# Kernel tuning notes

Hardware: AMD Instinct MI355X
Metric: run time of the kernel (lower is better)

Reference implementation:

```python
import jax, jax.numpy as jnp
import numpy as np

TEMPERATURE = 0.5
BN_EPS = 1e-5
L2_EPS = 1e-12

B, D_IN, D_HID, D_OUT = 4096, 192, 512, 128


def setup_inputs() -> dict:
    key = jax.random.key(0)
    ks = jax.random.split(key, 4)
    return {
        "h1": jax.random.normal(ks[0], (B, D_IN), dtype=jnp.float32),
        "h2": jax.random.normal(ks[1], (B, D_IN), dtype=jnp.float32),
        "W1": jax.random.normal(ks[2], (D_HID, D_IN), dtype=jnp.float32) * (1.0 / np.sqrt(D_IN)),
        "b1": jnp.zeros((D_HID,), dtype=jnp.float32),
        "gamma": jnp.ones((D_HID,), dtype=jnp.float32),
        "beta": jnp.zeros((D_HID,), dtype=jnp.float32),
        "W2": jax.random.normal(ks[3], (D_OUT, D_HID), dtype=jnp.float32) * (1.0 / np.sqrt(D_HID)),
        "b2": jnp.zeros((D_OUT,), dtype=jnp.float32),
    }


def _projection_head(h, W1, b1, gamma, beta, W2, b2):
    # Linear -> BatchNorm1d (training-mode batch stats) -> ReLU -> Linear
    y = h @ W1.T + b1  # (B, D_HID)
    mean = jnp.mean(y, axis=0)
    var = jnp.mean((y - mean) ** 2, axis=0)  # biased var, as torch BN uses for normalization
    y = (y - mean) * jax.lax.rsqrt(var + BN_EPS) * gamma + beta
    y = jax.nn.relu(y)
    return y @ W2.T + b2  # (B, D_OUT)


def _l2_normalize(z):
    n = jnp.sqrt(jnp.sum(z * z, axis=1, keepdims=True))
    return z / jnp.maximum(n, L2_EPS)


def reference(h1, h2, W1, b1, gamma, beta, W2, b2):
    z1 = _l2_normalize(_projection_head(h1, W1, b1, gamma, beta, W2, b2))
    z2 = _l2_normalize(_projection_head(h2, W1, b1, gamma, beta, W2, b2))

    # NT-Xent, fully vectorized (equivalent to the per-row torch loop):
    z = jnp.concatenate([z1, z2], axis=0)            # (2B, D)
    sim = (z @ z.T) / TEMPERATURE                    # (2B, 2B)
    n2 = z.shape[0]
    sim = jnp.where(jnp.eye(n2, dtype=bool), -jnp.inf, sim)
    # positive pair similarity: sim[i, i+B] and sim[i+B, i] == z1_i . z2_i / T
    pos = jnp.sum(z1 * z2, axis=1) / TEMPERATURE     # (B,)
    pos = jnp.concatenate([pos, pos])                # (2B,)
    # excluding index i from the row equals including it since diag is -inf
    lse = jax.nn.logsumexp(sim, axis=1)              # (2B,)
    loss = jnp.mean(lse - pos)
    return loss, z1, z2
```

## Files before the change

kernel.cpp:

```cpp
#include <hip/hip_runtime.h>


#define NB   4096
#define DIN  192
#define DHID 512
#define DOUT 128
#define N2   8192
#define NSPLIT 32
#define SIM_ITERS 16

typedef short short8 __attribute__((ext_vector_type(8)));
typedef float floatx4 __attribute__((ext_vector_type(4)));

__device__ inline float fast_exp2(float x) {
#if __has_builtin(__builtin_amdgcn_exp2f)
    return __builtin_amdgcn_exp2f(x);
#else
    return exp2f(x);
#endif
}

__device__ inline unsigned short bf16_rne(float x) {
    unsigned int u = __float_as_uint(x);
    return (unsigned short)((u + 0x7fffu + ((u >> 16) & 1u)) >> 16);
}

__global__ __launch_bounds__(256) void convert_w(
    const float* __restrict__ W1, const float* __restrict__ W2,
    unsigned short* __restrict__ W1b, unsigned short* __restrict__ W2b)
{
    const int NW1 = DHID * DIN / 4;
    const int NW2 = DOUT * DHID / 4;
    int id = blockIdx.x * 256 + threadIdx.x;
    const float* src; unsigned short* dst; int off;
    if (id < NW1)            { src = W1; dst = W1b; off = id; }
    else if (id < NW1 + NW2) { src = W2; dst = W2b; off = id - NW1; }
    else return;
    float4 x = ((const float4*)src)[off];
    unsigned int p0 = bf16_rne(x.x) | ((unsigned int)bf16_rne(x.y) << 16);
    unsigned int p1 = bf16_rne(x.z) | ((unsigned int)bf16_rne(x.w) << 16);
    ((uint2*)dst)[off] = make_uint2(p0, p1);
}

__global__ __launch_bounds__(256) void gemm1_mfma(
    const float* __restrict__ h1, const float* __restrict__ h2,
    const unsigned short* __restrict__ W1b, const float* __restrict__ b1,
    float* __restrict__ Y, float* __restrict__ psumc, float* __restrict__ psqc)
{
    const int t = threadIdx.x;
    const int wave = t >> 6, lane = t & 63;
    const int quad = lane >> 4, l15 = lane & 15;
    const int mb = blockIdx.x;
    const int m0 = mb * 128 + wave * 32;
    const int n0 = blockIdx.y * 64;
    const int v  = (mb >= 32);

    short8 a[2][6];
    #pragma unroll
    for (int mt = 0; mt < 2; ++mt) {
        int row = m0 + mt * 16 + l15;
        const float* hsrc = (row < NB) ? (h1 + (size_t)row * DIN)
                                       : (h2 + (size_t)(row - NB) * DIN);
        #pragma unroll
        for (int kc = 0; kc < 6; ++kc) {
            const float4* p = (const float4*)(hsrc + kc * 32 + quad * 8);
            float4 x0 = p[0], x1 = p[1];
            float xs[8] = {x0.x,x0.y,x0.z,x0.w,x1.x,x1.y,x1.z,x1.w};
            #pragma unroll
            for (int j = 0; j < 8; ++j) a[mt][kc][j] = (short)bf16_rne(xs[j]);
        }
    }

    #pragma unroll
    for (int nt = 0; nt < 4; ++nt) {
        const int col = n0 + nt * 16 + l15;
        const short8* bptr = (const short8*)(W1b + (size_t)col * DIN + quad * 8);
        short8 b[6];
        #pragma unroll
        for (int kc = 0; kc < 6; ++kc) b[kc] = bptr[kc * 4];
        floatx4 acc[2] = {{0.f,0.f,0.f,0.f},{0.f,0.f,0.f,0.f}};
        #pragma unroll
        for (int kc = 0; kc < 6; ++kc)
            #pragma unroll
            for (int mt = 0; mt < 2; ++mt)
                acc[mt] = __builtin_amdgcn_mfma_f32_16x16x32_bf16(a[mt][kc], b[kc], acc[mt], 0,0,0);
        const float bias = b1[col];
        float cs = 0.f, cq = 0.f;
        #pragma unroll
        for (int mt = 0; mt < 2; ++mt)
            #pragma unroll
            for (int reg = 0; reg < 4; ++reg) {
                float y = acc[mt][reg] + bias;
                int row = m0 + mt * 16 + quad * 4 + reg;
                Y[(size_t)row * DHID + col] = y;
                cs += y; cq += y * y;
            }
        cs += __shfl_xor(cs, 16); cs += __shfl_xor(cs, 32);
        cq += __shfl_xor(cq, 16); cq += __shfl_xor(cq, 32);
        if (quad == 0) {
            atomicAdd(psumc + v * DHID + col, cs);
            atomicAdd(psqc  + v * DHID + col, cq);
        }
    }
}

#define ZSCALE 1.6986436f

__global__ __launch_bounds__(256) void gemm2_mfma(
    const float* __restrict__ Y, const unsigned short* __restrict__ W2b,
    const float* __restrict__ psumc, const float* __restrict__ psqc,
    const float* __restrict__ gamma, const float* __restrict__ beta,
    const float* __restrict__ b2,
    unsigned short* __restrict__ Zb, float* __restrict__ outz)
{
    __shared__ float sc_sh[DHID], sh_sh[DHID];
    __shared__ float sq_lds[4][16];
    const int t = threadIdx.x;
    const int wave = t >> 6, lane = t & 63;
    const int quad = lane >> 4, l15 = lane & 15;
    const int mtbase = blockIdx.x * 16;
    const int v = (mtbase >= NB);

    for (int c = t; c < DHID; c += 256) {
        float mean = psumc[v * DHID + c] * (1.0f / NB);
        float var  = psqc [v * DHID + c] * (1.0f / NB) - mean * mean;
        float rstd = rsqrtf(var + 1e-5f);
        float scv = gamma[c] * rstd;
        sc_sh[c] = scv;
        sh_sh[c] = beta[c] - mean * scv;
    }
    __syncthreads();

    const float* yrow = Y + (size_t)(mtbase + l15) * DHID;
    floatx4 acc[2] = {{0.f,0.f,0.f,0.f},{0.f,0.f,0.f,0.f}};
    for (int kc = 0; kc < 16; ++kc) {
        const int k = kc * 32 + quad * 8;
        float4 y0 = *(const float4*)(yrow + k);
        float4 y1 = *(const float4*)(yrow + k + 4);
        float4 s0 = *(const float4*)&sc_sh[k], s1 = *(const float4*)&sc_sh[k + 4];
        float4 h0 = *(const float4*)&sh_sh[k], h1v = *(const float4*)&sh_sh[k + 4];
        float xs[8];
        xs[0] = fmaxf(y0.x * s0.x + h0.x, 0.f);
        xs[1] = fmaxf(y0.y * s0.y + h0.y, 0.f);
        xs[2] = fmaxf(y0.z * s0.z + h0.z, 0.f);
        xs[3] = fmaxf(y0.w * s0.w + h0.w, 0.f);
        xs[4] = fmaxf(y1.x * s1.x + h1v.x, 0.f);
        xs[5] = fmaxf(y1.y * s1.y + h1v.y, 0.f);
        xs[6] = fmaxf(y1.z * s1.z + h1v.z, 0.f);
        xs[7] = fmaxf(y1.w * s1.w + h1v.w, 0.f);
        short8 a;
        #pragma unroll
        for (int j = 0; j < 8; ++j) a[j] = (short)bf16_rne(xs[j]);
        #pragma unroll
        for (int nt = 0; nt < 2; ++nt) {
            const int col = wave * 32 + nt * 16 + l15;
            short8 b = *(const short8*)(W2b + (size_t)col * DHID + k);
            acc[nt] = __builtin_amdgcn_mfma_f32_16x16x32_bf16(a, b, acc[nt], 0,0,0);
        }
    }
    float bias[2];
    #pragma unroll
    for (int nt = 0; nt < 2; ++nt) bias[nt] = b2[wave * 32 + nt * 16 + l15];

    float zv[4][2];
    #pragma unroll
    for (int reg = 0; reg < 4; ++reg) {
        float sq = 0.f;
        #pragma unroll
        for (int nt = 0; nt < 2; ++nt) {
            zv[reg][nt] = acc[nt][reg] + bias[nt];
            sq += zv[reg][nt] * zv[reg][nt];
        }
        sq += __shfl_xor(sq, 1); sq += __shfl_xor(sq, 2);
        sq += __shfl_xor(sq, 4); sq += __shfl_xor(sq, 8);
        if (l15 == 0) sq_lds[wave][quad * 4 + reg] = sq;
    }
    __syncthreads();
    #pragma unroll
    for (int reg = 0; reg < 4; ++reg) {
        float tot = sq_lds[0][quad * 4 + reg] + sq_lds[1][quad * 4 + reg]
                  + sq_lds[2][quad * 4 + reg] + sq_lds[3][quad * 4 + reg];
        float inv = 1.0f / fmaxf(sqrtf(tot), 1e-12f);
        const int row = mtbase + quad * 4 + reg;
        const size_t ob = (size_t)row * DOUT;
        #pragma unroll
        for (int nt = 0; nt < 2; ++nt) {
            const int col = wave * 32 + nt * 16 + l15;
            float z = zv[reg][nt] * inv;
            outz[ob + col] = z;
            Zb[ob + col] = bf16_rne(z * ZSCALE);
        }
    }
}

__global__ __launch_bounds__(256, 2) void sim_mfma(
    const unsigned short* __restrict__ Zb, float* __restrict__ psum)
{
    __shared__ unsigned char bsh[65536];
    const int t = threadIdx.x;
    const int wave = t >> 6, lane = t & 63;
    const int quad = lane >> 4, l15 = lane & 15;
    const int mbase = blockIdx.x * 128 + wave * 32;
    const int cs = blockIdx.y;
    const int cbase = cs * (N2 / NSPLIT);

    {
        const uint4* src = (const uint4*)(Zb + (size_t)cbase * DOUT);
        #pragma unroll
        for (int k = 0; k < 16; ++k) {
            int idx = t + k * 256;
            uint4 vv = src[idx];
            int row  = idx >> 4;
            int slot = idx & 15;
            *(uint4*)(bsh + row * 256 + ((slot ^ (row & 15)) << 4)) = vv;
        }
    }

    short8 a[2][4];
    #pragma unroll
    for (int at = 0; at < 2; ++at) {
        const short8* zra = (const short8*)(Zb + (size_t)(mbase + at * 16 + l15) * DOUT + quad * 8);
        #pragma unroll
        for (int kc = 0; kc < 4; ++kc) a[at][kc] = zra[kc * 4];
    }

    float rs[2][4];
    #pragma unroll
    for (int at = 0; at < 2; ++at)
        #pragma unroll
        for (int r = 0; r < 4; ++r) rs[at][r] = 0.f;

    __syncthreads();

    #pragma unroll 1
    for (int nt = 0; nt < SIM_ITERS; ++nt) {
        const int crow = nt * 16 + l15;
        short8 b[4];
        #pragma unroll
        for (int kc = 0; kc < 4; ++kc) {
            int slot = kc * 4 + quad;
            int boff = crow * 256 + ((slot ^ (crow & 15)) << 4);
            b[kc] = *(const short8*)(bsh + boff);
        }

        floatx4 acc[2] = {{0.f,0.f,0.f,0.f},{0.f,0.f,0.f,0.f}};
        #pragma unroll
        for (int kc = 0; kc < 4; ++kc)
            #pragma unroll
            for (int at = 0; at < 2; ++at)
                acc[at] = __builtin_amdgcn_mfma_f32_16x16x32_bf16(a[at][kc], b[kc], acc[at], 0, 0, 0);

        #pragma unroll
        for (int at = 0; at < 2; ++at)
            #pragma unroll
            for (int r = 0; r < 4; ++r)
                rs[at][r] += fast_exp2(acc[at][r]);
    }

    #pragma unroll
    for (int at = 0; at < 2; ++at) {
        const int gi0 = mbase + at * 16 + quad * 4;
        #pragma unroll
        for (int r = 0; r < 4; ++r) {
            float s = rs[at][r];
            s += __shfl_xor(s, 1);
            s += __shfl_xor(s, 2);
            s += __shfl_xor(s, 4);
            s += __shfl_xor(s, 8);
            if (l15 == 0) psum[(size_t)cs * N2 + gi0 + r] = s;
        }
    }
}

__global__ __launch_bounds__(256) void row_finalize(
    const unsigned short* __restrict__ Zb, const float* __restrict__ psum,
    float* __restrict__ out)
{
    int i = blockIdx.x * 256 + threadIdx.x;
    float s = 0.f;
    #pragma unroll
    for (int cs = 0; cs < NSPLIT; ++cs) s += psum[(size_t)cs * N2 + i];
    int k = i & (NB - 1);
    const uint4* z1 = (const uint4*)(Zb + (size_t)k * DOUT);
    const uint4* z2 = (const uint4*)(Zb + (size_t)(k + NB) * DOUT);
    float d12 = 0.f, d11 = 0.f, d22 = 0.f;
    #pragma unroll
    for (int q = 0; q < 16; ++q) {
        uint4 a = z1[q], bqq = z2[q];
        const unsigned int aw[4] = {a.x, a.y, a.z, a.w};
        const unsigned int bw[4] = {bqq.x, bqq.y, bqq.z, bqq.w};
        #pragma unroll
        for (int c = 0; c < 4; ++c) {
            float alo = __uint_as_float(aw[c] << 16);
            float ahi = __uint_as_float(aw[c] & 0xffff0000u);
            float blo = __uint_as_float(bw[c] << 16);
            float bhi = __uint_as_float(bw[c] & 0xffff0000u);
            d12 += alo * blo + ahi * bhi;
            d11 += alo * alo + ahi * ahi;
            d22 += blo * blo + bhi * bhi;
        }
    }
    float dself = (i < NB) ? d11 : d22;
    float rowval = logf(s - fast_exp2(dself)) - d12 * 0.69314718f;

    float r = rowval;
    r += __shfl_xor(r, 1);  r += __shfl_xor(r, 2);  r += __shfl_xor(r, 4);
    r += __shfl_xor(r, 8);  r += __shfl_xor(r, 16); r += __shfl_xor(r, 32);
    __shared__ float wsr[4];
    int lane = threadIdx.x & 63, w = threadIdx.x >> 6;
    if (lane == 0) wsr[w] = r;
    __syncthreads();
    if (threadIdx.x == 0)
        atomicAdd(out, (wsr[0] + wsr[1] + wsr[2] + wsr[3]) * (1.0f / N2));
}

extern "C" void kernel_launch(void* const* d_in, const int* in_sizes, int n_in,
                              void* d_out, int out_size, void* d_ws, size_t ws_size,
                              hipStream_t stream)
{
    const float* h1    = (const float*)d_in[0];
    const float* h2    = (const float*)d_in[1];
    const float* W1    = (const float*)d_in[2];
    const float* b1    = (const float*)d_in[3];
    const float* gamma = (const float*)d_in[4];
    const float* beta  = (const float*)d_in[5];
    const float* W2    = (const float*)d_in[6];
    const float* b2    = (const float*)d_in[7];
    float* out = (float*)d_out;

    float* ws      = (float*)d_ws;
    float* psumc   = ws;
    float* psqc    = psumc + 1024;
    unsigned short* W1b = (unsigned short*)(psqc + 1024);
    unsigned short* W2b = W1b + DHID * DIN;
    float* Y       = (float*)(W2b + DOUT * DHID);
    float* psum    = Y + (size_t)N2 * DHID;
    unsigned short* Zb = (unsigned short*)(psum + (size_t)NSPLIT * N2);

    hipMemsetAsync(psumc, 0, 2048 * sizeof(float), stream);
    hipMemsetAsync(out, 0, sizeof(float), stream);

    convert_w   <<<dim3(160),        256, 0, stream>>>(W1, W2, W1b, W2b);
    gemm1_mfma  <<<dim3(64, 8),      256, 0, stream>>>(h1, h2, W1b, b1, Y, psumc, psqc);
    gemm2_mfma  <<<dim3(512),        256, 0, stream>>>(Y, W2b, psumc, psqc, gamma, beta, b2, Zb, out + 1);
    sim_mfma    <<<dim3(64, NSPLIT), 256, 0, stream>>>(Zb, psum);
    row_finalize<<<dim3(32),         256, 0, stream>>>(Zb, psum, out);
}
```

Baseline: 145.3 us.

## Fuse projection GEMMs into one cooperative kernel with grid sync for BN stats

Replaces the separate gemm1 and gemm2 launches with a single cooperative kernel. Each block computes a 16-row slice of the hidden activations into LDS, accumulates the BatchNorm column statistics atomically, grid-syncs, then applies BN, ReLU, the second GEMM and the L2 normalisation in place. This removes the round trip of the 8192x512 fp32 hidden activations through global memory and one launch. In exchange it needs all 512 blocks co-resident, adds a grid-wide barrier, and has each block recompute over a small tile with lower MFMA reuse of W1 and W2. If the cooperative launch fails it falls back to the old two-kernel path.

```diff
diff --git a/kernel.cpp b/kernel.cpp
--- a/kernel.cpp
+++ b/kernel.cpp
@@ -1,4 +1,5 @@
 #include <hip/hip_runtime.h>
+#include <hip/hip_cooperative_groups.h>
 
 
 #define NB   4096
@@ -42,6 +43,142 @@
     ((uint2*)dst)[off] = make_uint2(p0, p1);
 }
 
+#define ZSCALE 1.6986436f
+
+__global__ __launch_bounds__(256, 2) void fused_head(
+    const float* __restrict__ h1, const float* __restrict__ h2,
+    const unsigned short* __restrict__ W1b, const float* __restrict__ b1,
+    const unsigned short* __restrict__ W2b,
+    float* __restrict__ psumc, float* __restrict__ psqc,
+    const float* __restrict__ gamma, const float* __restrict__ beta,
+    const float* __restrict__ b2,
+    unsigned short* __restrict__ Zb, float* __restrict__ outz)
+{
+    __shared__ float ytile[16][516];
+    __shared__ float sc_sh[DHID], sh_sh[DHID];
+    __shared__ float sq_lds[4][16];
+
+    const int t = threadIdx.x;
+    const int wave = t >> 6, lane = t & 63;
+    const int quad = lane >> 4, l15 = lane & 15;
+    const int r0 = blockIdx.x * 16;
+    const int v  = (r0 >= NB);
+
+    {
+        short8 a1[6];
+        {
+            const int row = r0 + l15;
+            const float* hsrc = (row < NB) ? (h1 + (size_t)row * DIN)
+                                           : (h2 + (size_t)(row - NB) * DIN);
+            #pragma unroll
+            for (int kc = 0; kc < 6; ++kc) {
+                const float4* p = (const float4*)(hsrc + kc * 32 + quad * 8);
+                float4 x0 = p[0], x1 = p[1];
+                float xs[8] = {x0.x,x0.y,x0.z,x0.w,x1.x,x1.y,x1.z,x1.w};
+                #pragma unroll
+                for (int j = 0; j < 8; ++j) a1[kc][j] = (short)bf16_rne(xs[j]);
+            }
+        }
+        #pragma unroll
+        for (int nt = 0; nt < 8; ++nt) {
+            const int col = wave * 128 + nt * 16 + l15;
+            const short8* bptr = (const short8*)(W1b + (size_t)col * DIN + quad * 8);
+            floatx4 acc = {0.f, 0.f, 0.f, 0.f};
+            #pragma unroll
+            for (int kc = 0; kc < 6; ++kc)
+                acc = __builtin_amdgcn_mfma_f32_16x16x32_bf16(a1[kc], bptr[kc * 4], acc, 0, 0, 0);
+            const float bias = b1[col];
+            float cs = 0.f, cq = 0.f;
+            #pragma unroll
+            for (int reg = 0; reg < 4; ++reg) {
+                float y = acc[reg] + bias;
+                ytile[quad * 4 + reg][col] = y;
+                cs += y; cq += y * y;
+            }
+            cs += __shfl_xor(cs, 16); cs += __shfl_xor(cs, 32);
+            cq += __shfl_xor(cq, 16); cq += __shfl_xor(cq, 32);
+            if (quad == 0) {
+                atomicAdd(psumc + v * DHID + col, cs);
+                atomicAdd(psqc  + v * DHID + col, cq);
+            }
+        }
+    }
+    __threadfence();
+    cooperative_groups::this_grid().sync();
+
+    for (int c = t; c < DHID; c += 256) {
+        float sm = __hip_atomic_load(psumc + v * DHID + c, __ATOMIC_RELAXED, __HIP_MEMORY_SCOPE_AGENT);
+        float sq = __hip_atomic_load(psqc  + v * DHID + c, __ATOMIC_RELAXED, __HIP_MEMORY_SCOPE_AGENT);
+        float mean = sm * (1.0f / NB);
+        float var  = sq * (1.0f / NB) - mean * mean;
+        float rstd = rsqrtf(var + 1e-5f);
+        float scv = gamma[c] * rstd;
+        sc_sh[c] = scv;
+        sh_sh[c] = beta[c] - mean * scv;
+    }
+    __syncthreads();
+
+    floatx4 acc2[2] = {{0.f,0.f,0.f,0.f},{0.f,0.f,0.f,0.f}};
+    for (int kc = 0; kc < 16; ++kc) {
+        const int k = kc * 32 + quad * 8;
+        float4 y0 = *(const float4*)&ytile[l15][k];
+        float4 y1 = *(const float4*)&ytile[l15][k + 4];
+        float4 s0 = *(const float4*)&sc_sh[k], s1 = *(const float4*)&sc_sh[k + 4];
+        float4 h0 = *(const float4*)&sh_sh[k], h1v = *(const float4*)&sh_sh[k + 4];
+        float xs[8];
+        xs[0] = fmaxf(y0.x * s0.x + h0.x, 0.f);
+        xs[1] = fmaxf(y0.y * s0.y + h0.y, 0.f);
+        xs[2] = fmaxf(y0.z * s0.z + h0.z, 0.f);
+        xs[3] = fmaxf(y0.w * s0.w + h0.w, 0.f);
+        xs[4] = fmaxf(y1.x * s1.x + h1v.x, 0.f);
+        xs[5] = fmaxf(y1.y * s1.y + h1v.y, 0.f);
+        xs[6] = fmaxf(y1.z * s1.z + h1v.z, 0.f);
+        xs[7] = fmaxf(y1.w * s1.w + h1v.w, 0.f);
+        short8 a;
+        #pragma unroll
+        for (int j = 0; j < 8; ++j) a[j] = (short)bf16_rne(xs[j]);
+        #pragma unroll
+        for (int nt = 0; nt < 2; ++nt) {
+            const int col = wave * 32 + nt * 16 + l15;
+            short8 b = *(const short8*)(W2b + (size_t)col * DHID + k);
+            acc2[nt] = __builtin_amdgcn_mfma_f32_16x16x32_bf16(a, b, acc2[nt], 0, 0, 0);
+        }
+    }
+    float bias2[2];
+    #pragma unroll
+    for (int nt = 0; nt < 2; ++nt) bias2[nt] = b2[wave * 32 + nt * 16 + l15];
+
+    float zv[4][2];
+    #pragma unroll
+    for (int reg = 0; reg < 4; ++reg) {
+        float sq = 0.f;
+        #pragma unroll
+        for (int nt = 0; nt < 2; ++nt) {
+            zv[reg][nt] = acc2[nt][reg] + bias2[nt];
+            sq += zv[reg][nt] * zv[reg][nt];
+        }
+        sq += __shfl_xor(sq, 1); sq += __shfl_xor(sq, 2);
+        sq += __shfl_xor(sq, 4); sq += __shfl_xor(sq, 8);
+        if (l15 == 0) sq_lds[wave][quad * 4 + reg] = sq;
+    }
+    __syncthreads();
+    #pragma unroll
+    for (int reg = 0; reg < 4; ++reg) {
+        float tot = sq_lds[0][quad * 4 + reg] + sq_lds[1][quad * 4 + reg]
+                  + sq_lds[2][quad * 4 + reg] + sq_lds[3][quad * 4 + reg];
+        float inv = 1.0f / fmaxf(sqrtf(tot), 1e-12f);
+        const int row = r0 + quad * 4 + reg;
+        const size_t ob = (size_t)row * DOUT;
+        #pragma unroll
+        for (int nt = 0; nt < 2; ++nt) {
+            const int col = wave * 32 + nt * 16 + l15;
+            float z = zv[reg][nt] * inv;
+            outz[ob + col] = z;
+            Zb[ob + col] = bf16_rne(z * ZSCALE);
+        }
+    }
+}
+
 __global__ __launch_bounds__(256) void gemm1_mfma(
     const float* __restrict__ h1, const float* __restrict__ h2,
     const unsigned short* __restrict__ W1b, const float* __restrict__ b1,
@@ -103,8 +240,6 @@
         }
     }
 }
-
-#define ZSCALE 1.6986436f
 
 __global__ __launch_bounds__(256) void gemm2_mfma(
     const float* __restrict__ Y, const unsigned short* __restrict__ W2b,
@@ -341,8 +476,26 @@
     hipMemsetAsync(out, 0, sizeof(float), stream);
 
     convert_w   <<<dim3(160),        256, 0, stream>>>(W1, W2, W1b, W2b);
-    gemm1_mfma  <<<dim3(64, 8),      256, 0, stream>>>(h1, h2, W1b, b1, Y, psumc, psqc);
-    gemm2_mfma  <<<dim3(512),        256, 0, stream>>>(Y, W2b, psumc, psqc, gamma, beta, b2, Zb, out + 1);
+
+    {
+        const unsigned short* W1b_c = W1b;
+        const unsigned short* W2b_c = W2b;
+        unsigned short* Zb_p = Zb;
+        float* outz = out + 1;
+        void* args[] = {
+            (void*)&h1, (void*)&h2, (void*)&W1b_c, (void*)&b1, (void*)&W2b_c,
+            (void*)&psumc, (void*)&psqc, (void*)&gamma, (void*)&beta,
+            (void*)&b2, (void*)&Zb_p, (void*)&outz
+        };
+        hipError_t ce = hipLaunchCooperativeKernel((void*)fused_head,
+                                                   dim3(512), dim3(256),
+                                                   args, 0, stream);
+        if (ce != hipSuccess) {
+            gemm1_mfma<<<dim3(64, 8), 256, 0, stream>>>(h1, h2, W1b, b1, Y, psumc, psqc);
+            gemm2_mfma<<<dim3(512),   256, 0, stream>>>(Y, W2b, psumc, psqc, gamma, beta, b2, Zb, out + 1);
+        }
+    }
+
     sim_mfma    <<<dim3(64, NSPLIT), 256, 0, stream>>>(Zb, psum);
     row_finalize<<<dim3(32),         256, 0, stream>>>(Zb, psum, out);
 }
```

New measurement: 223.3 us. +53.6%, slower.
